# Kernel tuning notes

Hardware: AMD Instinct MI355X
Metric: run time of the kernel (lower is better)

The kernel has to match this reference:

```python
import jax, jax.numpy as jnp
import numpy as np

BN_EPS = 1e-5


def setup_inputs() -> dict:
    key = jax.random.key(0)
    ks = jax.random.split(key, 8)
    B, C, H, W = 8, 256, 48, 48
    s = 1.0 / np.sqrt(C)
    x = jax.random.normal(ks[0], (B, C, H, W), dtype=jnp.float32)
    Wk = jax.random.normal(ks[1], (C, C), dtype=jnp.float32) * s
    Wq = jax.random.normal(ks[2], (C, C), dtype=jnp.float32) * s
    Wv = jax.random.normal(ks[3], (C, C), dtype=jnp.float32) * s
    W2 = jax.random.normal(ks[4], (C, C), dtype=jnp.float32) * s
    b2 = jax.random.normal(ks[5], (C,), dtype=jnp.float32) * 0.02
    gamma = jnp.ones((C,), dtype=jnp.float32)
    beta = jnp.zeros((C,), dtype=jnp.float32)
    return {"x": x, "Wk": Wk, "Wq": Wq, "Wv": Wv, "W2": W2, "b2": b2,
            "gamma": gamma, "beta": beta}


def reference(x, Wk, Wq, Wv, W2, b2, gamma, beta):
    B, C, H, W = x.shape
    N = H * W
    xf = x.reshape(B, C, N)
    # 1x1 convs == channel mixing matmuls
    k = jnp.einsum('oc,bcn->bon', Wk, xf)  # (B,C,N)
    q = jnp.einsum('oc,bcn->bon', Wq, xf)  # (B,C,N)
    v = jnp.einsum('oc,bcn->bon', Wv, xf)  # (B,C,N)
    # scores[b,n,m] = sum_c k[b,c,n] * q[b,c,m]  (unscaled, as in source)
    scores = jnp.einsum('bcn,bcm->bnm', k, q)          # (B,N,N)
    prob = jax.nn.softmax(scores, axis=2)
    # out[b,c,n] = sum_m prob[b,n,m] * v[b,c,m]
    attn = jnp.einsum('bnm,bcm->bcn', prob, v).reshape(B, C, H, W)
    # react2: 1x1 conv (with bias) + BatchNorm2d (training-mode batch stats)
    y = jnp.einsum('oc,bchw->bohw', W2, attn) + b2[None, :, None, None]
    mean = jnp.mean(y, axis=(0, 2, 3))
    var = jnp.var(y, axis=(0, 2, 3))  # biased, matches torch BN normalization
    yhat = (y - mean[None, :, None, None]) * jax.lax.rsqrt(var + BN_EPS)[None, :, None, None]
    return yhat * gamma[None, :, None, None] + beta[None, :, None, None]
```

## Files before the change

### kernel.cpp

```cpp
#include <hip/hip_runtime.h>
#include <hip/hip_fp16.h>
#include <math.h>

#define BN_EPS 1e-5f

typedef unsigned short ushort_t;
typedef unsigned int uint_t;

constexpr int BB   = 8;
constexpr int CC   = 256;
constexpr int NN   = 2304;
constexpr int MTOT = BB * NN;
constexpr int NSPLIT = 4;
constexpr int MT32 = 72;
constexpr int TPS  = 18;
constexpr int TILE = 8192;
constexpr float MFIX = 64.0f;
constexpr size_t SZE = (size_t)BB * NN * CC;

typedef short bf16x8 __attribute__((ext_vector_type(8)));
typedef _Float16 f16x8 __attribute__((ext_vector_type(8)));
typedef float f32x16 __attribute__((ext_vector_type(16)));

union F4 { float4 v; float f[4]; };
union US4 { ushort_t u[4]; uint2 v; };
union U4H8 { uint4 v; ushort_t h[8]; };
union U4B8 { uint_t d[4]; bf16x8 v; };

__device__ __forceinline__ ushort_t f2bf(float f) {
  uint_t u = __float_as_uint(f);
  uint_t r = u + 0x7FFFu + ((u >> 16) & 1u);
  return (ushort_t)(r >> 16);
}
__device__ __forceinline__ float bf2f(ushort_t h) {
  return __uint_as_float(((uint_t)h) << 16);
}
__device__ __forceinline__ ushort_t f2h(float f) {
  return __half_as_ushort(__float2half(f));
}
__device__ __forceinline__ uint_t pk_trunc(float lo, float hi) {
  return __builtin_amdgcn_perm(__float_as_uint(hi), __float_as_uint(lo), 0x07060302u);
}
__device__ __forceinline__ int rowmap(int reg, int laneHi) {
  return (reg & 3) + 8 * (reg >> 2) + 4 * laneHi;
}

__global__ __launch_bounds__(256) void xpose(
    const float* __restrict__ x, ushort_t* __restrict__ xh, ushort_t* __restrict__ xl)
{
  const int b = blockIdx.z, n0 = blockIdx.y * 64, c0 = blockIdx.x * 64;
  __shared__ float t_s[64][67];
  const int tid = threadIdx.x;
#pragma unroll
  for (int t = 0; t < 4; ++t) {
    int e4 = tid + t * 256;
    int r = e4 >> 4, c4 = e4 & 15;
    F4 v; v.v = *(const float4*)&x[((size_t)b * CC + c0 + r) * NN + n0 + c4 * 4];
#pragma unroll
    for (int k = 0; k < 4; ++k) t_s[r][c4 * 4 + k] = v.f[k];
  }
  __syncthreads();
#pragma unroll
  for (int t = 0; t < 4; ++t) {
    int e = tid + t * 256;
    int nr = e >> 4, cc = e & 15;
    US4 hv, lv;
#pragma unroll
    for (int k = 0; k < 4; ++k) {
      const float v = t_s[cc * 4 + k][nr];
      const ushort_t h = f2bf(v);
      hv.u[k] = h;
      lv.u[k] = f2bf(v - bf2f(h));
    }
    const size_t o = ((size_t)b * NN + n0 + nr) * CC + c0 + cc * 4;
    *(uint2*)&xh[o] = hv.v;
    *(uint2*)&xl[o] = lv.v;
  }
}

__global__ __launch_bounds__(256) void wsplit(
    const float* __restrict__ Wk, const float* __restrict__ Wq,
    const float* __restrict__ Wv, const float* __restrict__ W2,
    ushort_t* __restrict__ wh, ushort_t* __restrict__ wl,
    float* __restrict__ stats)
{
  if (blockIdx.x < 2) stats[blockIdx.x * 256 + threadIdx.x] = 0.f;
  const int mat = blockIdx.x >> 5;
  const int off = ((blockIdx.x & 31) * 256 + threadIdx.x) * 8;
  const float* Wm = (mat == 0) ? Wk : (mat == 1) ? Wq : (mat == 2) ? Wv : W2;
  F4 a, c;
  a.v = *(const float4*)&Wm[off];
  c.v = *(const float4*)&Wm[off + 4];
  U4H8 hv, lv;
#pragma unroll
  for (int j = 0; j < 8; ++j) {
    const float v = (j < 4) ? a.f[j] : c.f[j - 4];
    const ushort_t h = f2bf(v);
    hv.h[j] = h;
    lv.h[j] = f2bf(v - bf2f(h));
  }
  *(uint4*)&wh[mat * 65536 + off] = hv.v;
  *(uint4*)&wl[mat * 65536 + off] = lv.v;
}

__global__ __launch_bounds__(256, 3) void qkv_mfma(
    const ushort_t* __restrict__ xh, const ushort_t* __restrict__ xl,
    const ushort_t* __restrict__ wh, const ushort_t* __restrict__ wl,
    ushort_t* __restrict__ kf, ushort_t* __restrict__ qf,
    ushort_t* __restrict__ vt2)
{
  const int mb  = blockIdx.x;
  const int mat = blockIdx.y >> 1;
  const int nh  = blockIdx.y & 1;
  const int b   = blockIdx.z;
  const int tid = threadIdx.x, w = tid >> 6, lane = tid & 63;
  const int l31 = lane & 31, lH = lane >> 5;
  const int wm = w & 1, wn = w >> 1;

  __shared__ alignas(16) ushort_t smem[24576];

  const size_t xrow = ((size_t)b * NN + mb * 64 + lane) * CC;
  const int obase = nh * 128;
  const size_t wrow = (size_t)(obase + lane) * CC;
  const ushort_t* whm = wh + mat * 65536;
  const ushort_t* wlm = wl + mat * 65536;

  f32x16 accA[2], accB[2], accC[2];
#pragma unroll
  for (int i = 0; i < 2; ++i) {
    accA[i] = (f32x16){}; accB[i] = (f32x16){}; accC[i] = (f32x16){};
  }

#define STAGE(k0)                                                                   \
  {                                                                                 \
    _Pragma("unroll")                                                               \
    for (int cc = 0; cc < 2; ++cc) {                                                \
      const int ch = 2 * w + cc;                                                    \
      const size_t gx = xrow + (k0) + ch * 8;                                       \
      __builtin_amdgcn_global_load_lds(                                             \
          (const __attribute__((address_space(1))) uint_t*)(xh + gx),               \
          (__attribute__((address_space(3))) uint_t*)(smem + ch * 512), 16, 0, 0);  \
      __builtin_amdgcn_global_load_lds(                                             \
          (const __attribute__((address_space(1))) uint_t*)(xl + gx),               \
          (__attribute__((address_space(3))) uint_t*)(smem + 4096 + ch * 512),      \
          16, 0, 0);                                                                \
      _Pragma("unroll")                                                             \
      for (int h = 0; h < 2; ++h) {                                                 \
        const size_t gw = wrow + (size_t)h * 64 * CC + (k0) + ch * 8;               \
        __builtin_amdgcn_global_load_lds(                                           \
            (const __attribute__((address_space(1))) uint_t*)(whm + gw),            \
            (__attribute__((address_space(3))) uint_t*)(smem + 8192 + ch * 1024 +   \
                                                        h * 512), 16, 0, 0);        \
        __builtin_amdgcn_global_load_lds(                                           \
            (const __attribute__((address_space(1))) uint_t*)(wlm + gw),            \
            (__attribute__((address_space(3))) uint_t*)(smem + 16384 + ch * 1024 +  \
                                                        h * 512), 16, 0, 0);        \
      }                                                                             \
    }                                                                               \
  }

#pragma unroll
  for (int t = 0; t < 4; ++t) {
    if (t) __syncthreads();
    STAGE(t * 64)
    __syncthreads();
#pragma unroll
    for (int kc = 0; kc < 4; ++kc) {
      const int ch = kc * 2 + lH;
      const bf16x8 Ah = *(const bf16x8*)&smem[(ch * 64 + wm * 32 + l31) * 8];
      const bf16x8 Al = *(const bf16x8*)&smem[4096 + (ch * 64 + wm * 32 + l31) * 8];
#pragma unroll
      for (int ot = 0; ot < 2; ++ot) {
        const int oL = wn * 64 + ot * 32 + l31;
        const bf16x8 Bh = *(const bf16x8*)&smem[8192 + (ch * 128 + oL) * 8];
        const bf16x8 Bl = *(const bf16x8*)&smem[16384 + (ch * 128 + oL) * 8];
        accA[ot] = __builtin_amdgcn_mfma_f32_32x32x16_bf16(Ah, Bh, accA[ot], 0, 0, 0);
        accB[ot] = __builtin_amdgcn_mfma_f32_32x32x16_bf16(Ah, Bl, accB[ot], 0, 0, 0);
        accC[ot] = __builtin_amdgcn_mfma_f32_32x32x16_bf16(Al, Bh, accC[ot], 0, 0, 0);
      }
    }
  }
#undef STAGE
  __syncthreads();

  ushort_t* vscr = smem + w * 1280;
  const int mt = mb * 2 + wm;
  const size_t tbase = (size_t)(b * MT32 + mt) * TILE;
#pragma unroll
  for (int ot = 0; ot < 2; ++ot) {
    const int o0 = obase + wn * 64 + ot * 32;
    if (mat < 2) {
#pragma unroll
      for (int reg = 0; reg < 16; ++reg)
        vscr[rowmap(reg, lH) * 40 + l31] =
            f2h(accA[ot][reg] + accB[ot][reg] + accC[ot][reg]);
      ushort_t* ob = ((mat == 0) ? kf : qf) + tbase;
#pragma unroll
      for (int k2 = 0; k2 < 2; ++k2) {
        const int idx = k2 * 64 + lane;
        const int n = idx >> 2, coct = idx & 3;
        uint4 pk = *(const uint4*)&vscr[n * 40 + coct * 8];
        *(uint4*)&ob[(size_t)(((o0 >> 3) + coct) * 32 + n) * 8] = pk;
      }
    } else {
#pragma unroll
      for (int reg = 0; reg < 16; ++reg)
        vscr[l31 * 40 + rowmap(reg, lH)] =
            f2bf(accA[ot][reg] + accB[ot][reg] + accC[ot][reg]);
#pragma unroll
      for (int k2 = 0; k2 < 2; ++k2) {
        const int idx = k2 * 64 + lane;
        const int cl = idx >> 2, moct = idx & 3;
        uint4 pk = *(const uint4*)&vscr[cl * 40 + moct * 8];
        *(uint4*)&vt2[tbase + (size_t)(moct * 256 + o0 + cl) * 8] = pk;
      }
    }
  }
}

__global__ __launch_bounds__(256, 2) void attn_fused(
    const ushort_t* __restrict__ kf, const ushort_t* __restrict__ qf,
    const ushort_t* __restrict__ vt2,
    ushort_t* __restrict__ Opart, float* __restrict__ Ls)
{
  const int id = blockIdx.x + 18 * (blockIdx.y + 4 * blockIdx.z);
  const int xcd = id & 7, s = id >> 3;
  const int g = xcd * 4 + s / 18;
  const int n0 = (s % 18) * 128;
  const int split = g & 3, b = g >> 2;

  const int tid = threadIdx.x;
  const int w = tid >> 6, lane = tid & 63;
  const int l31 = lane & 31, lH = lane >> 5;

  __shared__ alignas(16) ushort_t sQ[2 * TILE];
  __shared__ alignas(16) ushort_t sV[2 * TILE];

  const ushort_t* qtb = qf + (size_t)(b * MT32 + split * TPS) * TILE;
  const ushort_t* vtb = vt2 + (size_t)(b * MT32 + split * TPS) * TILE;

  f16x8 Kf[16];
  {
    const ushort_t* kt = kf + (size_t)(b * MT32 + (n0 >> 5) + w) * TILE;
#pragma unroll
    for (int kc = 0; kc < 16; ++kc)
      Kf[kc] = *(const f16x8*)&kt[(size_t)((kc * 2 + lH) * 32 + l31) * 8];
  }
  f32x16 O[8];
#pragma unroll
  for (int i = 0; i < 8; ++i) O[i] = (f32x16){};
  float rsum = 0.f;

#define ISSUE_TILE(tt, buf)                                                        \
  {                                                                                \
    const ushort_t* qs = qtb + (size_t)(tt) * TILE;                                \
    const ushort_t* vs = vtb + (size_t)(tt) * TILE;                                \
    ushort_t* ldq = sQ + (buf) * TILE;                                             \
    ushort_t* ldv = sV + (buf) * TILE;                                             \
    _Pragma("unroll")                                                              \
    for (int j = 0; j < 4; ++j) {                                                  \
      const int i = w * 4 + j;                                                     \
      __builtin_amdgcn_global_load_lds(                                            \
          (const __attribute__((address_space(1))) uint_t*)(qs + i * 512 + lane * 8), \
          (__attribute__((address_space(3))) uint_t*)(ldq + i * 512), 16, 0, 0);   \
      __builtin_amdgcn_global_load_lds(                                            \
          (const __attribute__((address_space(1))) uint_t*)(vs + i * 512 + lane * 8), \
          (__attribute__((address_space(3))) uint_t*)(ldv + i * 512), 16, 0, 0);   \
    }                                                                              \
  }

  ISSUE_TILE(0, 0)
  ISSUE_TILE(1, 1)
  __syncthreads();

  for (int t = 0; t < TPS; ++t) {
    const int cur = t & 1;
    const ushort_t* Qs = sQ + cur * TILE;
    const ushort_t* Vs = sV + cur * TILE;
    f32x16 acc = {};
    __builtin_amdgcn_s_setprio(1);
#pragma unroll
    for (int kc = 0; kc < 16; ++kc) {
      f16x8 Aq = *(const f16x8*)&Qs[(size_t)((kc * 2 + lH) * 32 + l31) * 8];
      acc = __builtin_amdgcn_mfma_f32_32x32x16_f16(Aq, Kf[kc], acc, 0, 0, 0);
    }
    __builtin_amdgcn_s_setprio(0);
    float p[16];
#pragma unroll
    for (int r = 0; r < 16; ++r) p[r] = __expf(acc[r] - MFIX);
#pragma unroll
    for (int g4 = 0; g4 < 4; ++g4)
      rsum += (p[4 * g4] + p[4 * g4 + 1]) + (p[4 * g4 + 2] + p[4 * g4 + 3]);
    uint_t dA0 = pk_trunc(p[0], p[1]),   dB0 = pk_trunc(p[2], p[3]);
    uint_t dA1 = pk_trunc(p[4], p[5]),   dB1 = pk_trunc(p[6], p[7]);
    uint_t dA2 = pk_trunc(p[8], p[9]),   dB2 = pk_trunc(p[10], p[11]);
    uint_t dA3 = pk_trunc(p[12], p[13]), dB3 = pk_trunc(p[14], p[15]);
    asm volatile("v_permlane32_swap_b32 %0, %1" : "+v"(dA0), "+v"(dA1));
    asm volatile("v_permlane32_swap_b32 %0, %1" : "+v"(dB0), "+v"(dB1));
    asm volatile("v_permlane32_swap_b32 %0, %1" : "+v"(dA2), "+v"(dA3));
    asm volatile("v_permlane32_swap_b32 %0, %1" : "+v"(dB2), "+v"(dB3));
    U4B8 fr0, fr1;
    fr0.d[0] = dA0; fr0.d[1] = dB0; fr0.d[2] = dA1; fr0.d[3] = dB1;
    fr1.d[0] = dA2; fr1.d[1] = dB2; fr1.d[2] = dA3; fr1.d[3] = dB3;
#pragma unroll
    for (int ks = 0; ks < 2; ++ks) {
      const bf16x8 Bp = ks ? fr1.v : fr0.v;
      __builtin_amdgcn_s_setprio(1);
#pragma unroll
      for (int cg = 0; cg < 8; ++cg) {
        bf16x8 Av = *(const bf16x8*)&Vs[(size_t)((ks * 2 + lH) * 256 + cg * 32 + l31) * 8];
        O[cg] = __builtin_amdgcn_mfma_f32_32x32x16_bf16(Av, Bp, O[cg], 0, 0, 0);
      }
      __builtin_amdgcn_s_setprio(0);
    }
    __syncthreads();
    if (t + 2 < TPS) ISSUE_TILE(t + 2, cur)
  }
#undef ISSUE_TILE

  ushort_t* Ob = Opart + (size_t)(split * BB + b) * CC * NN;
  const int n = n0 + w * 32 + l31;
#pragma unroll
  for (int cg = 0; cg < 8; ++cg)
#pragma unroll
    for (int reg = 0; reg < 16; ++reg) {
      const int c = cg * 32 + rowmap(reg, lH);
      Ob[(size_t)c * NN + n] = f2bf(O[cg][reg]);
    }
  rsum += __shfl_xor(rsum, 32);
  if (lH == 0)
    Ls[(size_t)split * MTOT + b * NN + n] = rsum;
}

__global__ __launch_bounds__(256, 2) void proj_f(
    const ushort_t* __restrict__ Opart, const float* __restrict__ Ls,
    const ushort_t* __restrict__ w2h, const ushort_t* __restrict__ w2l,
    const float* __restrict__ b2,
    ushort_t* __restrict__ yb, float* __restrict__ stats)
{
  const int mt = blockIdx.x;
  const int tid = threadIdx.x, w = tid >> 6, lane = tid & 63;
  const int l31 = lane & 31, lH = lane >> 5, h8 = lH * 8;
  const int r0 = mt * 32;
  const int b = r0 / NN, nb = r0 % NN;

  __shared__ alignas(16) ushort_t t_s[32 * 264];
  __shared__ float inv_s[32];

  if (tid < 32) {
    float L = 0.f;
#pragma unroll
    for (int sp = 0; sp < NSPLIT; ++sp) L += Ls[(size_t)sp * MTOT + r0 + tid];
    inv_s[tid] = 1.0f / L;
  }
  __syncthreads();

  const size_t obase = ((size_t)b * CC) * NN + nb;
#pragma unroll
  for (int k = 0; k < 4; ++k) {
    const int c = (tid >> 2) + k * 64;
    const int noct = tid & 3;
    float accv[8] = {};
#pragma unroll
    for (int sp = 0; sp < NSPLIT; ++sp) {
      U4H8 pk;
      pk.v = *(const uint4*)&Opart[(size_t)sp * SZE + obase + (size_t)c * NN + noct * 8];
#pragma unroll
      for (int j = 0; j < 8; ++j) accv[j] += bf2f(pk.h[j]);
    }
#pragma unroll
    for (int j = 0; j < 8; ++j) {
      const int nl = noct * 8 + j;
      t_s[nl * 264 + c] = f2bf(accv[j] * inv_s[nl]);
    }
  }
  __syncthreads();

  bf16x8 Af[16];
#pragma unroll
  for (int kc = 0; kc < 16; ++kc)
    Af[kc] = *(const bf16x8*)&t_s[l31 * 264 + kc * 16 + h8];

#pragma unroll
  for (int ot = 0; ot < 2; ++ot) {
    const int o0 = w * 64 + ot * 32;
    f32x16 accA = {}, accB = {};
#pragma unroll
    for (int kc = 0; kc < 16; ++kc) {
      bf16x8 Bh = *(const bf16x8*)&w2h[(size_t)(o0 + l31) * CC + kc * 16 + h8];
      bf16x8 Bl = *(const bf16x8*)&w2l[(size_t)(o0 + l31) * CC + kc * 16 + h8];
      accA = __builtin_amdgcn_mfma_f32_32x32x16_bf16(Af[kc], Bh, accA, 0, 0, 0);
      accB = __builtin_amdgcn_mfma_f32_32x32x16_bf16(Af[kc], Bl, accB, 0, 0, 0);
    }
    const float bj = b2[o0 + l31];
    float cs = 0.f, cq = 0.f;
#pragma unroll
    for (int reg = 0; reg < 16; ++reg) {
      const float v = accA[reg] + accB[reg] + bj;
      yb[(size_t)(r0 + rowmap(reg, lH)) * CC + o0 + l31] = f2bf(v);
      cs += v;
      cq += v * v;
    }
    cs += __shfl_xor(cs, 32);
    cq += __shfl_xor(cq, 32);
    if (lane < 32) {
      atomicAdd(&stats[o0 + l31], cs);
      atomicAdd(&stats[CC + o0 + l31], cq);
    }
  }
}

__global__ __launch_bounds__(256) void bn_out(
    const ushort_t* __restrict__ yb, const float* __restrict__ stats,
    const float* __restrict__ gamma, const float* __restrict__ beta,
    float* __restrict__ out)
{
  const int b = blockIdx.z, n0 = blockIdx.y * 64, c0 = blockIdx.x * 64;
  __shared__ alignas(16) ushort_t t_s[64 * 72];
  __shared__ float aa[64], bbf[64];
  const int tid = threadIdx.x;
  if (tid < 64) {
    const int c = c0 + tid;
    const float mean = stats[c] * (1.0f / MTOT);
    const float var  = stats[CC + c] * (1.0f / MTOT) - mean * mean;
    const float rstd = rsqrtf(var + BN_EPS);
    const float a = rstd * gamma[c];
    aa[tid]  = a;
    bbf[tid] = beta[c] - mean * a;
  }
#pragma unroll
  for (int t = 0; t < 2; ++t) {
    const int e = tid + t * 256;
    const int r = e >> 3, c8 = e & 7;
    const int sc8 = c8 ^ (r & 7);
    *(uint4*)&t_s[r * 72 + sc8 * 8] =
        *(const uint4*)&yb[((size_t)b * NN + n0 + r) * CC + c0 + c8 * 8];
  }
  __syncthreads();
#pragma unroll
  for (int t = 0; t < 4; ++t) {
    const int e4 = tid + t * 256;
    const int cr = e4 >> 4, r4 = e4 & 15;
    const float a = aa[cr], bb2 = bbf[cr];
    F4 o4;
#pragma unroll
    for (int k = 0; k < 4; ++k) {
      const int r = r4 * 4 + k;
      const int idx = r * 72 + (((cr >> 3) ^ (r & 7)) << 3) + (cr & 7);
      o4.f[k] = bf2f(t_s[idx]) * a + bb2;
    }
    *(float4*)&out[((size_t)b * CC + c0 + cr) * NN + n0 + r4 * 4] = o4.v;
  }
}

extern "C" void kernel_launch(void* const* d_in, const int* in_sizes, int n_in,
                              void* d_out, int out_size, void* d_ws, size_t ws_size,
                              hipStream_t stream)
{
  (void)in_sizes; (void)n_in; (void)out_size; (void)ws_size;
  const float* x     = (const float*)d_in[0];
  const float* Wk    = (const float*)d_in[1];
  const float* Wq    = (const float*)d_in[2];
  const float* Wv    = (const float*)d_in[3];
  const float* W2    = (const float*)d_in[4];
  const float* b2    = (const float*)d_in[5];
  const float* gamma = (const float*)d_in[6];
  const float* beta  = (const float*)d_in[7];
  float* out = (float*)d_out;

  ushort_t* u   = (ushort_t*)d_ws;
  ushort_t* xh  = u;
  ushort_t* xl  = u + SZE;
  ushort_t* kf  = u + 2 * SZE;
  ushort_t* qf  = u + 3 * SZE;
  ushort_t* vt2 = u + 4 * SZE;
  ushort_t* Opart = u + 5 * SZE;
  ushort_t* wh  = u + (5 + NSPLIT) * SZE;
  ushort_t* wl  = wh + 4 * 65536;
  float* Ls    = (float*)(wl + 4 * 65536);
  float* stats = Ls + (size_t)NSPLIT * MTOT;
  ushort_t* yb = u;

  xpose     <<<dim3(4, 36, 8),       256, 0, stream>>>(x, xh, xl);
  wsplit    <<<dim3(128),            256, 0, stream>>>(Wk, Wq, Wv, W2, wh, wl, stats);
  qkv_mfma  <<<dim3(36, 6, 8),       256, 0, stream>>>(xh, xl, wh, wl, kf, qf, vt2);
  attn_fused<<<dim3(18, NSPLIT, 8),  256, 0, stream>>>(kf, qf, vt2, Opart, Ls);
  proj_f    <<<dim3(576),            256, 0, stream>>>(Opart, Ls, wh + 3 * 65536,
                                                       wl + 3 * 65536, b2, yb, stats);
  bn_out    <<<dim3(4, 36, 8),       256, 0, stream>>>(yb, stats, gamma, beta, out);
}
```

Before: 245.6 us.

## Double-buffer QKV projection LDS staging with smaller K chunks

The QKV projection GEMM now stages x and weight tiles into two alternating LDS buffers, using 32-wide K chunks over 8 iterations instead of 64-wide chunks over 4. The next-but-one chunk is issued right after the barrier, so global-to-LDS loads overlap with MFMA work on the other buffer. This aims to hide global load latency and remove one barrier per step. The trade-offs are more loop iterations, and any vmcnt wait the compiler puts before each barrier may serialize the loads and limit the overlap.

```diff
diff --git a/kernel.cpp b/kernel.cpp
--- a/kernel.cpp
+++ b/kernel.cpp
@@ -121,7 +121,6 @@
 
   const size_t xrow = ((size_t)b * NN + mb * 64 + lane) * CC;
   const int obase = nh * 128;
-  const size_t wrow = (size_t)(obase + lane) * CC;
   const ushort_t* whm = wh + mat * 65536;
   const ushort_t* wlm = wl + mat * 65536;
 
@@ -131,57 +130,55 @@
     accA[i] = (f32x16){}; accB[i] = (f32x16){}; accC[i] = (f32x16){};
   }
 
-#define STAGE(k0)                                                                   \
+#define STAGE(k0, bf)                                                               \
   {                                                                                 \
+    ushort_t* bb = smem + (bf) * 12288;                                             \
+    __builtin_amdgcn_global_load_lds(                                               \
+        (const __attribute__((address_space(1))) uint_t*)(xh + xrow + (k0) + w * 8),\
+        (__attribute__((address_space(3))) uint_t*)(bb + w * 512), 16, 0, 0);       \
+    __builtin_amdgcn_global_load_lds(                                               \
+        (const __attribute__((address_space(1))) uint_t*)(xl + xrow + (k0) + w * 8),\
+        (__attribute__((address_space(3))) uint_t*)(bb + 2048 + w * 512), 16, 0, 0);\
     _Pragma("unroll")                                                               \
-    for (int cc = 0; cc < 2; ++cc) {                                                \
-      const int ch = 2 * w + cc;                                                    \
-      const size_t gx = xrow + (k0) + ch * 8;                                       \
+    for (int h = 0; h < 2; ++h) {                                                   \
+      const size_t gw = (size_t)(obase + h * 64 + lane) * CC + (k0) + w * 8;        \
       __builtin_amdgcn_global_load_lds(                                             \
-          (const __attribute__((address_space(1))) uint_t*)(xh + gx),               \
-          (__attribute__((address_space(3))) uint_t*)(smem + ch * 512), 16, 0, 0);  \
+          (const __attribute__((address_space(1))) uint_t*)(whm + gw),              \
+          (__attribute__((address_space(3))) uint_t*)(bb + 4096 + w * 1024 +        \
+                                                      h * 512), 16, 0, 0);          \
       __builtin_amdgcn_global_load_lds(                                             \
-          (const __attribute__((address_space(1))) uint_t*)(xl + gx),               \
-          (__attribute__((address_space(3))) uint_t*)(smem + 4096 + ch * 512),      \
-          16, 0, 0);                                                                \
-      _Pragma("unroll")                                                             \
-      for (int h = 0; h < 2; ++h) {                                                 \
-        const size_t gw = wrow + (size_t)h * 64 * CC + (k0) + ch * 8;               \
-        __builtin_amdgcn_global_load_lds(                                           \
-            (const __attribute__((address_space(1))) uint_t*)(whm + gw),            \
-            (__attribute__((address_space(3))) uint_t*)(smem + 8192 + ch * 1024 +   \
-                                                        h * 512), 16, 0, 0);        \
-        __builtin_amdgcn_global_load_lds(                                           \
-            (const __attribute__((address_space(1))) uint_t*)(wlm + gw),            \
-            (__attribute__((address_space(3))) uint_t*)(smem + 16384 + ch * 1024 +  \
-                                                        h * 512), 16, 0, 0);        \
-      }                                                                             \
+          (const __attribute__((address_space(1))) uint_t*)(wlm + gw),              \
+          (__attribute__((address_space(3))) uint_t*)(bb + 8192 + w * 1024 +        \
+                                                      h * 512), 16, 0, 0);          \
     }                                                                               \
   }
 
-#pragma unroll
-  for (int t = 0; t < 4; ++t) {
-    if (t) __syncthreads();
-    STAGE(t * 64)
-    __syncthreads();
-#pragma unroll
-    for (int kc = 0; kc < 4; ++kc) {
-      const int ch = kc * 2 + lH;
-      const bf16x8 Ah = *(const bf16x8*)&smem[(ch * 64 + wm * 32 + l31) * 8];
-      const bf16x8 Al = *(const bf16x8*)&smem[4096 + (ch * 64 + wm * 32 + l31) * 8];
+  STAGE(0, 0)
+  __syncthreads();
+  STAGE(32, 1)
+
+#pragma unroll
+  for (int t = 0; t < 8; ++t) {
+    const ushort_t* bb = smem + (t & 1) * 12288;
+#pragma unroll
+    for (int kc2 = 0; kc2 < 2; ++kc2) {
+      const int ch = kc2 * 2 + lH;
+      const bf16x8 Ah = *(const bf16x8*)&bb[(ch * 64 + wm * 32 + l31) * 8];
+      const bf16x8 Al = *(const bf16x8*)&bb[2048 + (ch * 64 + wm * 32 + l31) * 8];
 #pragma unroll
       for (int ot = 0; ot < 2; ++ot) {
         const int oL = wn * 64 + ot * 32 + l31;
-        const bf16x8 Bh = *(const bf16x8*)&smem[8192 + (ch * 128 + oL) * 8];
-        const bf16x8 Bl = *(const bf16x8*)&smem[16384 + (ch * 128 + oL) * 8];
+        const bf16x8 Bh = *(const bf16x8*)&bb[4096 + (ch * 128 + oL) * 8];
+        const bf16x8 Bl = *(const bf16x8*)&bb[8192 + (ch * 128 + oL) * 8];
         accA[ot] = __builtin_amdgcn_mfma_f32_32x32x16_bf16(Ah, Bh, accA[ot], 0, 0, 0);
         accB[ot] = __builtin_amdgcn_mfma_f32_32x32x16_bf16(Ah, Bl, accB[ot], 0, 0, 0);
         accC[ot] = __builtin_amdgcn_mfma_f32_32x32x16_bf16(Al, Bh, accC[ot], 0, 0, 0);
       }
     }
+    __syncthreads();
+    if (t + 2 < 8) STAGE((t + 2) * 32, t & 1)
   }
 #undef STAGE
-  __syncthreads();
 
   ushort_t* vscr = smem + w * 1280;
   const int mt = mb * 2 + wm;
```

New measurement: 241.8 us (median of 2 runs). About the same (-1.5%).
